# Optimization experiments

Measured on AMD Instinct MI355X. Metric: run time of the kernel, lower is better.

The kernel has to match this reference:

```python
import jax, jax.numpy as jnp
import numpy as np

N, IN_F, OUT_F = 8192, 512, 256
NEG_INF = -9e15
LEAKY_SLOPE = 0.25


def setup_inputs() -> dict:
    key = jax.random.key(0)
    k1, k2, k3, k4, k5, k6 = jax.random.split(key, 6)
    inp = {
        "input": jax.random.normal(k1, (N, IN_F), dtype=jnp.float32),
        "adj": jax.random.randint(k2, (N, N), 0, 2, dtype=jnp.int32),
        # learned params (xavier-normal-ish scale)
        "weights": jax.random.normal(k3, (IN_F, OUT_F), dtype=jnp.float32) * (2.0 / (IN_F + OUT_F)) ** 0.5,
        "a1": jax.random.normal(k4, (OUT_F, 1), dtype=jnp.float32) * (2.0 / (OUT_F + 1)) ** 0.5,
        "a2": jax.random.normal(k5, (OUT_F, 1), dtype=jnp.float32) * (2.0 / (OUT_F + 1)) ** 0.5,
        "bias": jax.random.uniform(k6, (OUT_F,), dtype=jnp.float32, minval=-1.0 / OUT_F ** 0.5, maxval=1.0 / OUT_F ** 0.5),
    }
    return inp


def reference(input, adj, weights, a1, a2, bias):
    # h = input @ W  : [N, out]
    h = input @ weights
    # e[i,j] = leaky_relu((h@a1)[i] + (h@a2)[j])  : [N, N] via broadcast
    e1 = h @ a1  # [N,1]
    e2 = h @ a2  # [N,1]
    e = e1 + e2.T
    e = jnp.where(e > 0, e, LEAKY_SLOPE * e)
    # mask non-edges, row softmax (dropout omitted: deterministic reference)
    scores = jnp.where(adj > 0, e, NEG_INF)
    attention = jax.nn.softmax(scores, axis=1)
    # aggregate + bias
    return attention @ h + bias
```

## Files before the change

### kernel.cpp

```cpp
#include <hip/hip_runtime.h>
#include <hip/hip_fp16.h>

typedef __attribute__((ext_vector_type(8))) short short8;
typedef __attribute__((ext_vector_type(4))) float floatx4;
typedef __attribute__((ext_vector_type(4))) unsigned int uintx4;
typedef __attribute__((ext_vector_type(2))) unsigned int uintx2;
typedef __attribute__((ext_vector_type(4))) int intx4;
typedef __attribute__((ext_vector_type(4))) unsigned short ushortx4;
typedef unsigned int u32;

#define NN 8192
#define KIN 512
#define COUT 256
#define SHIFT 16.0f

#define AS1 __attribute__((address_space(1)))
#define AS3 __attribute__((address_space(3)))

__device__ __forceinline__ void stage16(const void* g, void* l) {
  __builtin_amdgcn_global_load_lds((const AS1 u32*)g, (AS3 u32*)l, 16, 0, 0);
}

__device__ __forceinline__ unsigned int f2bf(float f) {
  unsigned int u = __float_as_uint(f);
  return (u + 0x7FFFu + ((u >> 16) & 1u)) >> 16;
}

__device__ __forceinline__ u32 pkbf(float lo, float hi) {
  u32 a = __float_as_uint(lo) + 0x8000u;
  u32 b = __float_as_uint(hi) + 0x8000u;
  return __builtin_amdgcn_perm(b, a, 0x07060302u);
}

__device__ __forceinline__ short8 pack8(const float* p) {
  uintx4 w;
  w.x = pkbf(p[0], p[1]);
  w.y = pkbf(p[2], p[3]);
  w.z = pkbf(p[4], p[5]);
  w.w = pkbf(p[6], p[7]);
  union { uintx4 u; short8 s; } cv; cv.u = w;
  return cv.s;
}

__global__ void k_cast_input(const float* __restrict__ in, ushortx4* __restrict__ out) {
  int idx = blockIdx.x * 256 + threadIdx.x;
  floatx4 v = ((const floatx4*)in)[idx];
  ushortx4 o;
  o.x = (unsigned short)f2bf(v.x);
  o.y = (unsigned short)f2bf(v.y);
  o.z = (unsigned short)f2bf(v.z);
  o.w = (unsigned short)f2bf(v.w);
  out[idx] = o;
}

__global__ void k_prep_w(const float* __restrict__ w, unsigned short* __restrict__ wt) {
  int idx = blockIdx.x * 256 + threadIdx.x;
  int k = idx >> 8, c = idx & 255;
  wt[c * KIN + k] = (unsigned short)f2bf(w[idx]);
}

__global__ __launch_bounds__(256)
void k_gemm_h(const unsigned short* __restrict__ inA, const unsigned short* __restrict__ wt,
              const float* __restrict__ a1, const float* __restrict__ a2,
              unsigned short* __restrict__ ht, float* __restrict__ e1, float* __restrict__ e2,
              float* __restrict__ A1, float* __restrict__ A2, u32* __restrict__ e2pk) {
  int wave = threadIdx.x >> 6;
  int lane = threadIdx.x & 63;
  int n = lane & 15, q = lane >> 4;
  int row0 = blockIdx.x * 64 + wave * 16;
  int mrow = row0 + n;

  floatx4 acc[16];
#pragma unroll
  for (int t = 0; t < 16; ++t) acc[t] = (floatx4){0.f, 0.f, 0.f, 0.f};

  for (int kc = 0; kc < KIN / 32; ++kc) {
    int k0 = kc * 32 + q * 8;
    short8 a = *(const short8*)(inA + (size_t)mrow * KIN + k0);
#pragma unroll
    for (int nt = 0; nt < 16; ++nt) {
      short8 b = *(const short8*)(wt + (size_t)(nt * 16 + n) * KIN + k0);
      acc[nt] = __builtin_amdgcn_mfma_f32_16x16x32_bf16(a, b, acc[nt], 0, 0, 0);
    }
  }

  int i0 = row0 + q * 4;
#pragma unroll
  for (int nt = 0; nt < 16; ++nt) {
    int c = nt * 16 + n;
    uintx2 pk;
    pk.x = f2bf(acc[nt][0]) | (f2bf(acc[nt][1]) << 16);
    pk.y = f2bf(acc[nt][2]) | (f2bf(acc[nt][3]) << 16);
    *(uintx2*)(ht + (size_t)c * NN + i0) = pk;
  }

  float s1[4] = {0.f, 0.f, 0.f, 0.f}, s2[4] = {0.f, 0.f, 0.f, 0.f};
#pragma unroll
  for (int nt = 0; nt < 16; ++nt) {
    float w1 = a1[nt * 16 + n];
    float w2 = a2[nt * 16 + n];
#pragma unroll
    for (int r = 0; r < 4; ++r) {
      s1[r] += acc[nt][r] * w1;
      s2[r] += acc[nt][r] * w2;
    }
  }
#pragma unroll
  for (int m = 1; m < 16; m <<= 1) {
#pragma unroll
    for (int r = 0; r < 4; ++r) {
      s1[r] += __shfl_xor(s1[r], m);
      s2[r] += __shfl_xor(s2[r], m);
    }
  }
  if (n == 0) {
#pragma unroll
    for (int r = 0; r < 4; ++r) {
      float v1 = s1[r], v2 = s2[r];
      e1[i0 + r] = v1;
      e2[i0 + r] = v2;
      A1[i0 + r] = __expf(v1 - 8.0f);
      A2[i0 + r] = __expf(0.25f * v1 - 8.0f);
      u32 b1 = f2bf(__expf(v2 - 8.0f));
      u32 b2 = f2bf(__expf(0.25f * v2 - 8.0f));
      e2pk[i0 + r] = (b1 << 16) | b2;
    }
  }
}

__global__ __launch_bounds__(256, 2)
void k_attn_fused(const int* __restrict__ adj, const unsigned short* __restrict__ ht,
                  const float* __restrict__ A1, const float* __restrict__ A2,
                  const u32* __restrict__ e2pk,
                  __half2* __restrict__ oph, float* __restrict__ Dpart) {
  __shared__ __align__(16) char smem[69632];
  u32* e2s = (u32*)(smem + 65536);

  int b = blockIdx.x;
  int rg = b >> 3, js = b & 7;
  int wave = threadIdx.x >> 6, lane = threadIdx.x & 63;
  int n = lane & 15, q = lane >> 4;
  int rowblock = rg * 128;
  int rowbase = rowblock + wave * 32;
  int jbeg = js * 1024;

  ((uintx4*)e2s)[threadIdx.x] = *(const uintx4*)(e2pk + jbeg + threadIdx.x * 4);

  float A1v0 = A1[rowbase + n],      A2v0 = A2[rowbase + n];
  float A1v1 = A1[rowbase + 16 + n], A2v1 = A2[rowbase + 16 + n];

  floatx4 acc[2][16];
  floatx4 accd[2];
#pragma unroll
  for (int t = 0; t < 2; ++t) {
    accd[t] = (floatx4){0.f, 0.f, 0.f, 0.f};
#pragma unroll
    for (int nt = 0; nt < 16; ++nt) acc[t][nt] = (floatx4){0.f, 0.f, 0.f, 0.f};
  }

  union { uintx4 u; short8 s; } onesu;
  onesu.u = (uintx4){0x3F803F80u, 0x3F803F80u, 0x3F803F80u, 0x3F803F80u};
  short8 ones = onesu.s;

  auto stage = [&](int ch, int buf) {
    int j0g = jbeg + ch * 32;
    char* hbase = smem + buf * 32768;
#pragma unroll
    for (int i = 0; i < 4; ++i) {
      int seg = wave * 256 + i * 64 + lane;
      int c = seg >> 2;
      int j8 = (seg & 3) * 8;
      stage16(ht + (size_t)c * NN + j0g + j8, hbase + (size_t)(wave * 256 + i * 64) * 16);
    }
    char* abase = hbase + 16384 + wave * 4096;
    const int* aw = adj + (size_t)(rowblock + wave * 32) * NN + j0g;
#pragma unroll
    for (int i = 0; i < 4; ++i) {
      stage16(aw + (size_t)(i * 8 + (lane & 7)) * NN + (lane >> 3) * 4, abase + i * 1024);
    }
  };

  int rlo = n & 7, rhi = n >> 3;

  stage(0, 0);
  asm volatile("s_waitcnt lgkmcnt(0)" ::: "memory");
  asm volatile("s_barrier" ::: "memory");

  for (int ch = 0; ch < 32; ++ch) {
    int cur = ch & 1;
    if (ch < 31) {
      stage(ch + 1, cur ^ 1);
      asm volatile("s_waitcnt vmcnt(8)" ::: "memory");
    } else {
      asm volatile("s_waitcnt vmcnt(0)" ::: "memory");
    }

    const char* ab = smem + cur * 32768 + 16384 + wave * 4096;
    intx4 a0a = *(const intx4*)(ab + rhi * 1024 + q * 256 + rlo * 16);
    intx4 a0b = *(const intx4*)(ab + rhi * 1024 + q * 256 + 128 + rlo * 16);
    intx4 a1a = *(const intx4*)(ab + 2048 + rhi * 1024 + q * 256 + rlo * 16);
    intx4 a1b = *(const intx4*)(ab + 2048 + rhi * 1024 + q * 256 + 128 + rlo * 16);

    uintx4 ba = *(const uintx4*)(e2s + ch * 32 + q * 8);
    uintx4 bb = *(const uintx4*)(e2s + ch * 32 + q * 8 + 4);
    u32 bw[8] = {ba.x, ba.y, ba.z, ba.w, bb.x, bb.y, bb.z, bb.w};

    float p0[8], p1[8];
#pragma unroll
    for (int jj = 0; jj < 8; ++jj) {
      int av0 = (jj < 4) ? a0a[jj] : a0b[jj - 4];
      int av1 = (jj < 4) ? a1a[jj] : a1b[jj - 4];
      float B1 = __uint_as_float(bw[jj] & 0xffff0000u);
      float B2 = __uint_as_float(bw[jj] << 16);
      float m10 = A1v0 * B1, m20 = A2v0 * B2;
      float m11 = A1v1 * B1, m21 = A2v1 * B2;
      float pm0 = fmaxf(m10, m20);
      float pm1 = fmaxf(m11, m21);
      p0[jj] = (av0 != 0) ? pm0 : 0.f;
      p1[jj] = (av1 != 0) ? pm1 : 0.f;
    }
    short8 af0 = pack8(p0);
    short8 af1 = pack8(p1);

    asm volatile("s_barrier" ::: "memory");

    const short8* lb = (const short8*)(smem + (size_t)cur * 32768);
#pragma unroll
    for (int t = 0; t < 16; ++t) {
      short8 bf = lb[t * 64 + n * 4 + q];
      acc[0][t] = __builtin_amdgcn_mfma_f32_16x16x32_bf16(af0, bf, acc[0][t], 0, 0, 0);
      acc[1][t] = __builtin_amdgcn_mfma_f32_16x16x32_bf16(af1, bf, acc[1][t], 0, 0, 0);
    }
    accd[0] = __builtin_amdgcn_mfma_f32_16x16x32_bf16(af0, ones, accd[0], 0, 0, 0);
    accd[1] = __builtin_amdgcn_mfma_f32_16x16x32_bf16(af1, ones, accd[1], 0, 0, 0);

    asm volatile("s_waitcnt lgkmcnt(0)" ::: "memory");
    asm volatile("s_barrier" ::: "memory");
  }

  if (n == 0) {
#pragma unroll
    for (int t2 = 0; t2 < 2; ++t2)
#pragma unroll
      for (int r = 0; r < 4; ++r)
        Dpart[(size_t)js * NN + rowbase + t2 * 16 + q * 4 + r] = accd[t2][r];
  }

#pragma unroll
  for (int t2 = 0; t2 < 2; ++t2) {
    int ibase = rowbase + t2 * 16 + q * 4;
#pragma unroll
    for (int nt = 0; nt < 16; ++nt) {
      int c = nt * 16 + n;
      oph[((size_t)js * 4096 + (ibase >> 1)) * 256 + c] =
          __floats2half2_rn(acc[t2][nt][0], acc[t2][nt][1]);
      oph[((size_t)js * 4096 + (ibase >> 1) + 1) * 256 + c] =
          __floats2half2_rn(acc[t2][nt][2], acc[t2][nt][3]);
    }
  }
}

__global__ void k_final_part(float* __restrict__ out, const __half2* __restrict__ oph,
                             const float* __restrict__ Dpart, const float* __restrict__ bias) {
  int i = blockIdx.x;
  int c = threadIdx.x;
  int hi = i & 1;
  float s = 0.f, d = 0.f;
#pragma unroll
  for (int js = 0; js < 8; ++js) {
    __half2 h2 = oph[((size_t)js * 4096 + (i >> 1)) * 256 + c];
    s += hi ? __high2float(h2) : __low2float(h2);
    d += Dpart[(size_t)js * NN + i];
  }
  out[(size_t)i * COUT + c] = s / fmaxf(d, 1e-37f) + bias[c];
}

__global__ __launch_bounds__(256, 2)
void k_attn_atomic(const int* __restrict__ adj, const unsigned short* __restrict__ ht,
                   const float* __restrict__ e1, const float* __restrict__ e2,
                   float* __restrict__ out_num, float* __restrict__ Dbuf) {
  int b = blockIdx.x;
  int rg = b >> 3, js = b & 7;
  int wave = threadIdx.x >> 6, lane = threadIdx.x & 63;
  int n = lane & 15, q = lane >> 4;
  int rowbase = rg * 128 + wave * 32;

  float e1v0 = e1[rowbase + n];
  float e1v1 = e1[rowbase + 16 + n];

  floatx4 acc[2][16];
#pragma unroll
  for (int t = 0; t < 2; ++t)
#pragma unroll
    for (int nt = 0; nt < 16; ++nt) acc[t][nt] = (floatx4){0.f, 0.f, 0.f, 0.f};

  float d0 = 0.f, d1 = 0.f;
  int jbeg = js * 1024;

  for (int ch = 0; ch < 32; ++ch) {
    int j0 = jbeg + ch * 32 + q * 8;
    floatx4 ea = *(const floatx4*)(e2 + j0);
    floatx4 eb = *(const floatx4*)(e2 + j0 + 4);
    float ev[8] = {ea.x, ea.y, ea.z, ea.w, eb.x, eb.y, eb.z, eb.w};

    intx4 A00 = *(const intx4*)(adj + (size_t)(rowbase + n) * NN + j0);
    intx4 A01 = *(const intx4*)(adj + (size_t)(rowbase + n) * NN + j0 + 4);
    intx4 A10 = *(const intx4*)(adj + (size_t)(rowbase + 16 + n) * NN + j0);
    intx4 A11 = *(const intx4*)(adj + (size_t)(rowbase + 16 + n) * NN + j0 + 4);

    float p0[8], p1[8];
#pragma unroll
    for (int jj = 0; jj < 8; ++jj) {
      int av0 = (jj < 4) ? A00[jj] : A01[jj - 4];
      int av1 = (jj < 4) ? A10[jj] : A11[jj - 4];
      float t0 = e1v0 + ev[jj];
      float t1 = e1v1 + ev[jj];
      float f0 = fmaxf(t0, 0.25f * t0);
      float f1 = fmaxf(t1, 0.25f * t1);
      float x0 = __expf(f0 - SHIFT);
      float x1 = __expf(f1 - SHIFT);
      p0[jj] = (av0 != 0) ? x0 : 0.f;
      p1[jj] = (av1 != 0) ? x1 : 0.f;
      d0 += p0[jj];
      d1 += p1[jj];
    }
    short8 af0 = pack8(p0);
    short8 af1 = pack8(p1);

#pragma unroll
    for (int g = 0; g < 2; ++g) {
      short8 bf[8];
#pragma unroll
      for (int t = 0; t < 8; ++t)
        bf[t] = *(const short8*)(ht + (size_t)((g * 8 + t) * 16 + n) * NN + j0);
#pragma unroll
      for (int t = 0; t < 8; ++t) {
        acc[0][g * 8 + t] = __builtin_amdgcn_mfma_f32_16x16x32_bf16(af0, bf[t], acc[0][g * 8 + t], 0, 0, 0);
        acc[1][g * 8 + t] = __builtin_amdgcn_mfma_f32_16x16x32_bf16(af1, bf[t], acc[1][g * 8 + t], 0, 0, 0);
      }
    }
  }

  d0 += __shfl_xor(d0, 16); d0 += __shfl_xor(d0, 32);
  d1 += __shfl_xor(d1, 16); d1 += __shfl_xor(d1, 32);
  if (lane < 16) {
    atomicAdd(Dbuf + rowbase + lane, d0);
    atomicAdd(Dbuf + rowbase + 16 + lane, d1);
  }

#pragma unroll
  for (int t2 = 0; t2 < 2; ++t2) {
#pragma unroll
    for (int nt = 0; nt < 16; ++nt) {
#pragma unroll
      for (int r = 0; r < 4; ++r) {
        int i = rowbase + t2 * 16 + q * 4 + r;
        atomicAdd(out_num + (size_t)i * COUT + nt * 16 + n, acc[t2][nt][r]);
      }
    }
  }
}

__global__ void k_final_atomic(float* __restrict__ out, const float* __restrict__ Dbuf,
                               const float* __restrict__ bias) {
  int idx = blockIdx.x * 256 + threadIdx.x;
  int i = idx >> 8, c = idx & 255;
  float d = fmaxf(Dbuf[i], 1e-37f);
  out[idx] = out[idx] / d + bias[c];
}

extern "C" void kernel_launch(void* const* d_in, const int* in_sizes, int n_in,
                              void* d_out, int out_size, void* d_ws, size_t ws_size,
                              hipStream_t stream) {
  const float* input   = (const float*)d_in[0];
  const int*   adj     = (const int*)d_in[1];
  const float* weights = (const float*)d_in[2];
  const float* a1      = (const float*)d_in[3];
  const float* a2      = (const float*)d_in[4];
  const float* bias    = (const float*)d_in[5];
  float* out = (float*)d_out;
  char* ws = (char*)d_ws;

  unsigned short* inA = (unsigned short*)(ws);
  unsigned short* wt  = (unsigned short*)(ws + 8388608);
  unsigned short* ht  = (unsigned short*)(ws + 8650752);
  float* e1    = (float*)(ws + 12845056);
  float* e2    = (float*)(ws + 12877824);
  float* A1    = (float*)(ws + 12910592);
  float* A2    = (float*)(ws + 12943360);
  u32*   e2pk  = (u32*)  (ws + 12976128);
  float* Dpart = (float*)(ws + 13008896);
  __half2* oph = (__half2*)(ws + 13271040);
  const size_t WS_NEEDED_PART = 13271040 + (size_t)8 * NN * COUT * 2;
  float* Dbuf = Dpart;

  k_cast_input<<<4096, 256, 0, stream>>>(input, (ushortx4*)inA);
  k_prep_w<<<512, 256, 0, stream>>>(weights, wt);
  k_gemm_h<<<128, 256, 0, stream>>>(inA, wt, a1, a2, ht, e1, e2, A1, A2, e2pk);

  if (ws_size >= WS_NEEDED_PART) {
    k_attn_fused<<<512, 256, 0, stream>>>(adj, ht, A1, A2, e2pk, oph, Dpart);
    k_final_part<<<8192, 256, 0, stream>>>(out, oph, Dpart, bias);
  } else {
    hipMemsetAsync(out, 0, (size_t)NN * COUT * sizeof(float), stream);
    hipMemsetAsync(Dbuf, 0, NN * sizeof(float), stream);
    k_attn_atomic<<<512, 256, 0, stream>>>(adj, ht, e1, e2, out, Dbuf);
    k_final_atomic<<<8192, 256, 0, stream>>>(out, Dbuf, bias);
  }
}
```

Before: 447.7 us.

## Halve attention block row tile to raise occupancy to three blocks per CU

Each attention block now processes 64 rows (16 per wave) instead of 128, with smaller LDS buffers and a single accumulator set per wave. The grid doubles and launch bounds target three blocks per CU, aiming for more latency hiding on the adjacency stream. In exchange, every block reloads the shared h tile, which doubles h traffic and halves MFMA operand reuse. The larger grid also may not divide evenly across CUs.

Result: slower. 462.2 us (+3.2%).

```diff
diff --git a/kernel.cpp b/kernel.cpp
--- a/kernel.cpp
+++ b/kernel.cpp
@@ -128,35 +128,30 @@
   }
 }
 
-__global__ __launch_bounds__(256, 2)
+__global__ __launch_bounds__(256, 3)
 void k_attn_fused(const int* __restrict__ adj, const unsigned short* __restrict__ ht,
                   const float* __restrict__ A1, const float* __restrict__ A2,
                   const u32* __restrict__ e2pk,
                   __half2* __restrict__ oph, float* __restrict__ Dpart) {
-  __shared__ __align__(16) char smem[69632];
-  u32* e2s = (u32*)(smem + 65536);
+  __shared__ __align__(16) char smem[53248];
+  u32* e2s = (u32*)(smem + 49152);
 
   int b = blockIdx.x;
   int rg = b >> 3, js = b & 7;
   int wave = threadIdx.x >> 6, lane = threadIdx.x & 63;
   int n = lane & 15, q = lane >> 4;
-  int rowblock = rg * 128;
-  int rowbase = rowblock + wave * 32;
+  int rowblock = rg * 64;
+  int rowbase = rowblock + wave * 16;
   int jbeg = js * 1024;
 
   ((uintx4*)e2s)[threadIdx.x] = *(const uintx4*)(e2pk + jbeg + threadIdx.x * 4);
 
-  float A1v0 = A1[rowbase + n],      A2v0 = A2[rowbase + n];
-  float A1v1 = A1[rowbase + 16 + n], A2v1 = A2[rowbase + 16 + n];
-
-  floatx4 acc[2][16];
-  floatx4 accd[2];
-#pragma unroll
-  for (int t = 0; t < 2; ++t) {
-    accd[t] = (floatx4){0.f, 0.f, 0.f, 0.f};
-#pragma unroll
-    for (int nt = 0; nt < 16; ++nt) acc[t][nt] = (floatx4){0.f, 0.f, 0.f, 0.f};
-  }
+  float A1v = A1[rowbase + n], A2v = A2[rowbase + n];
+
+  floatx4 acc[16];
+  floatx4 accd = (floatx4){0.f, 0.f, 0.f, 0.f};
+#pragma unroll
+  for (int nt = 0; nt < 16; ++nt) acc[nt] = (floatx4){0.f, 0.f, 0.f, 0.f};
 
   union { uintx4 u; short8 s; } onesu;
   onesu.u = (uintx4){0x3F803F80u, 0x3F803F80u, 0x3F803F80u, 0x3F803F80u};
@@ -164,7 +159,7 @@
 
   auto stage = [&](int ch, int buf) {
     int j0g = jbeg + ch * 32;
-    char* hbase = smem + buf * 32768;
+    char* hbase = smem + buf * 16384;
 #pragma unroll
     for (int i = 0; i < 4; ++i) {
       int seg = wave * 256 + i * 64 + lane;
@@ -172,10 +167,10 @@
       int j8 = (seg & 3) * 8;
       stage16(ht + (size_t)c * NN + j0g + j8, hbase + (size_t)(wave * 256 + i * 64) * 16);
     }
-    char* abase = hbase + 16384 + wave * 4096;
-    const int* aw = adj + (size_t)(rowblock + wave * 32) * NN + j0g;
-#pragma unroll
-    for (int i = 0; i < 4; ++i) {
+    char* abase = smem + 32768 + buf * 8192 + wave * 2048;
+    const int* aw = adj + (size_t)(rowblock + wave * 16) * NN + j0g;
+#pragma unroll
+    for (int i = 0; i < 2; ++i) {
       stage16(aw + (size_t)(i * 8 + (lane & 7)) * NN + (lane >> 3) * 4, abase + i * 1024);
     }
   };
@@ -190,49 +185,39 @@
     int cur = ch & 1;
     if (ch < 31) {
       stage(ch + 1, cur ^ 1);
-      asm volatile("s_waitcnt vmcnt(8)" ::: "memory");
+      asm volatile("s_waitcnt vmcnt(6)" ::: "memory");
     } else {
       asm volatile("s_waitcnt vmcnt(0)" ::: "memory");
     }
 
-    const char* ab = smem + cur * 32768 + 16384 + wave * 4096;
+    const char* ab = smem + 32768 + cur * 8192 + wave * 2048;
     intx4 a0a = *(const intx4*)(ab + rhi * 1024 + q * 256 + rlo * 16);
     intx4 a0b = *(const intx4*)(ab + rhi * 1024 + q * 256 + 128 + rlo * 16);
-    intx4 a1a = *(const intx4*)(ab + 2048 + rhi * 1024 + q * 256 + rlo * 16);
-    intx4 a1b = *(const intx4*)(ab + 2048 + rhi * 1024 + q * 256 + 128 + rlo * 16);
 
     uintx4 ba = *(const uintx4*)(e2s + ch * 32 + q * 8);
     uintx4 bb = *(const uintx4*)(e2s + ch * 32 + q * 8 + 4);
     u32 bw[8] = {ba.x, ba.y, ba.z, ba.w, bb.x, bb.y, bb.z, bb.w};
 
-    float p0[8], p1[8];
+    float p0[8];
 #pragma unroll
     for (int jj = 0; jj < 8; ++jj) {
       int av0 = (jj < 4) ? a0a[jj] : a0b[jj - 4];
-      int av1 = (jj < 4) ? a1a[jj] : a1b[jj - 4];
       float B1 = __uint_as_float(bw[jj] & 0xffff0000u);
       float B2 = __uint_as_float(bw[jj] << 16);
-      float m10 = A1v0 * B1, m20 = A2v0 * B2;
-      float m11 = A1v1 * B1, m21 = A2v1 * B2;
-      float pm0 = fmaxf(m10, m20);
-      float pm1 = fmaxf(m11, m21);
+      float pm0 = fmaxf(A1v * B1, A2v * B2);
       p0[jj] = (av0 != 0) ? pm0 : 0.f;
-      p1[jj] = (av1 != 0) ? pm1 : 0.f;
     }
     short8 af0 = pack8(p0);
-    short8 af1 = pack8(p1);
 
     asm volatile("s_barrier" ::: "memory");
 
-    const short8* lb = (const short8*)(smem + (size_t)cur * 32768);
+    const short8* lb = (const short8*)(smem + (size_t)cur * 16384);
 #pragma unroll
     for (int t = 0; t < 16; ++t) {
       short8 bf = lb[t * 64 + n * 4 + q];
-      acc[0][t] = __builtin_amdgcn_mfma_f32_16x16x32_bf16(af0, bf, acc[0][t], 0, 0, 0);
-      acc[1][t] = __builtin_amdgcn_mfma_f32_16x16x32_bf16(af1, bf, acc[1][t], 0, 0, 0);
-    }
-    accd[0] = __builtin_amdgcn_mfma_f32_16x16x32_bf16(af0, ones, accd[0], 0, 0, 0);
-    accd[1] = __builtin_amdgcn_mfma_f32_16x16x32_bf16(af1, ones, accd[1], 0, 0, 0);
+      acc[t] = __builtin_amdgcn_mfma_f32_16x16x32_bf16(af0, bf, acc[t], 0, 0, 0);
+    }
+    accd = __builtin_amdgcn_mfma_f32_16x16x32_bf16(af0, ones, accd, 0, 0, 0);
 
     asm volatile("s_waitcnt lgkmcnt(0)" ::: "memory");
     asm volatile("s_barrier" ::: "memory");
@@ -240,23 +225,18 @@
 
   if (n == 0) {
 #pragma unroll
-    for (int t2 = 0; t2 < 2; ++t2)
-#pragma unroll
-      for (int r = 0; r < 4; ++r)
-        Dpart[(size_t)js * NN + rowbase + t2 * 16 + q * 4 + r] = accd[t2][r];
-  }
-
-#pragma unroll
-  for (int t2 = 0; t2 < 2; ++t2) {
-    int ibase = rowbase + t2 * 16 + q * 4;
-#pragma unroll
-    for (int nt = 0; nt < 16; ++nt) {
-      int c = nt * 16 + n;
-      oph[((size_t)js * 4096 + (ibase >> 1)) * 256 + c] =
-          __floats2half2_rn(acc[t2][nt][0], acc[t2][nt][1]);
-      oph[((size_t)js * 4096 + (ibase >> 1) + 1) * 256 + c] =
-          __floats2half2_rn(acc[t2][nt][2], acc[t2][nt][3]);
-    }
+    for (int r = 0; r < 4; ++r)
+      Dpart[(size_t)js * NN + rowbase + q * 4 + r] = accd[r];
+  }
+
+  int ibase = rowbase + q * 4;
+#pragma unroll
+  for (int nt = 0; nt < 16; ++nt) {
+    int c = nt * 16 + n;
+    oph[((size_t)js * 4096 + (ibase >> 1)) * 256 + c] =
+        __floats2half2_rn(acc[nt][0], acc[nt][1]);
+    oph[((size_t)js * 4096 + (ibase >> 1) + 1) * 256 + c] =
+        __floats2half2_rn(acc[nt][2], acc[nt][3]);
   }
 }
 
@@ -399,7 +379,7 @@
   k_gemm_h<<<128, 256, 0, stream>>>(inA, wt, a1, a2, ht, e1, e2, A1, A2, e2pk);
 
   if (ws_size >= WS_NEEDED_PART) {
-    k_attn_fused<<<512, 256, 0, stream>>>(adj, ht, A1, A2, e2pk, oph, Dpart);
+    k_attn_fused<<<1024, 256, 0, stream>>>(adj, ht, A1, A2, e2pk, oph, Dpart);
     k_final_part<<<8192, 256, 0, stream>>>(out, oph, Dpart, bias);
   } else {
     hipMemsetAsync(out, 0, (size_t)NN * COUT * sizeof(float), stream);
```
